# Kernel tuning notes

Measured on AMD Instinct MI355X. Metric: run time of the kernel, lower is better.

The kernel has to match this reference:

```python
import jax, jax.numpy as jnp
import numpy as np

EPS = 1e-6
MAX_ITER = 3

def skew(w):
    z = jnp.zeros_like(w[:, 0])
    return jnp.stack([
        jnp.stack([z, -w[:, 2], w[:, 1]], -1),
        jnp.stack([w[:, 2], z, -w[:, 0]], -1),
        jnp.stack([-w[:, 1], w[:, 0], z], -1)], -2)

def twist2mat(w):
    # Rodrigues formula, w: [B,3] -> R: [B,3,3]
    theta = jnp.linalg.norm(w, axis=-1, keepdims=True) + 1e-12
    axis = w / theta
    Km = skew(axis)
    th = theta[..., None]
    I = jnp.eye(3, dtype=w.dtype)
    return I + jnp.sin(th) * Km + (1.0 - jnp.cos(th)) * (Km @ Km)

def sobel_gradient(img, normalize=True):
    # replicate-pad + 3x3 Sobel, img: [B,C,H,W]
    p = jnp.pad(img, ((0, 0), (0, 0), (1, 1), (1, 1)), mode='edge')
    tl = p[..., :-2, :-2]; tc = p[..., :-2, 1:-1]; tr = p[..., :-2, 2:]
    ml = p[..., 1:-1, :-2]; mr = p[..., 1:-1, 2:]
    bl = p[..., 2:, :-2]; bc = p[..., 2:, 1:-1]; br = p[..., 2:, 2:]
    dx = (tr - tl) + 2.0 * (mr - ml) + (br - bl)
    dy = (bl - tl) + 2.0 * (bc - tc) + (br - tr)
    if normalize:
        mag = jnp.sqrt(dx * dx + dy * dy + 1e-8)
        dx, dy = dx / mag, dy / mag
    return dx, dy

def _bilinear_one(F, u, v):
    # F: [C,H,W]; u,v: [H,W] pixel coords; border padding (grid_sample-like)
    C, H, W = F.shape
    u = jnp.clip(u, 0.0, W - 1.0)
    v = jnp.clip(v, 0.0, H - 1.0)
    x0 = jnp.floor(u); y0 = jnp.floor(v)
    wx = u - x0; wy = v - y0
    x0i = x0.astype(jnp.int32); y0i = y0.astype(jnp.int32)
    x1i = jnp.minimum(x0i + 1, W - 1); y1i = jnp.minimum(y0i + 1, H - 1)
    g = lambda yi, xi: F[:, yi, xi]  # advanced-index gather -> [C,H,W]
    return (g(y0i, x0i) * (1 - wx) * (1 - wy) + g(y0i, x1i) * wx * (1 - wy)
            + g(y1i, x0i) * (1 - wx) * wy + g(y1i, x1i) * wx * wy)

def warp_features(F, u, v):
    # F: [B,C,H,W]; u,v: [B,1,H,W]
    return jax.vmap(_bilinear_one)(F, u[:, 0], v[:, 0])

def generate_xy_grid(B, H, W, K):
    fx, fy, cx, cy = [K[:, i].reshape(B, 1, 1, 1) for i in range(4)]
    uu, vv = jnp.meshgrid(jnp.arange(W, dtype=K.dtype), jnp.arange(H, dtype=K.dtype))
    px = (uu[None, None] - cx) / fx
    py = (vv[None, None] - cy) / fy
    return px, py  # [B,1,H,W] each

def batch_warp_inverse_depth(px, py, invD0, R, t, K):
    B, _, H, W = px.shape
    xy1 = jnp.concatenate([px, py, jnp.ones_like(px)], 1).reshape(B, 3, -1)
    warped = R @ xy1 + t[:, :, None] * invD0.reshape(B, 1, -1)
    x_, y_, s_ = warped[:, 0], warped[:, 1], warped[:, 2]
    fx, fy, cx, cy = [K[:, i].reshape(B, 1) for i in range(4)]
    u_ = (x_ / s_ * fx + cx).reshape(B, 1, H, W)
    v_ = (y_ / s_ * fy + cy).reshape(B, 1, H, W)
    inv_z = invD0 / s_.reshape(B, 1, H, W)
    return u_, v_, inv_z

def check_occ(inv_z_buffer, invD1, u, v, thres=0.1):
    B, _, H, W = invD1.shape
    inv_z_warped = warp_features(invD1, u, v)
    inlier = inv_z_buffer > inv_z_warped - thres
    inview = (u > 0) & (u < W) & (v > 0) & (v < H)
    return ~(inlier & inview)  # [B,1,H,W] bool

def compute_jacobian_warping(invD, K, px, py):
    # linearized at origin (pose=None branch)
    B, _, H, W = invD.shape
    x = px.reshape(B, -1); y = py.reshape(B, -1); d = invD.reshape(B, -1)
    O = jnp.zeros_like(x)
    xy = x * y
    dx_dp = jnp.stack([-xy, 1.0 + x * x, -y, d, O, -d * x], -1)
    dy_dp = jnp.stack([-(1.0 + y * y), xy, x, O, d, -d * y], -1)
    fx = K[:, 0].reshape(B, 1, 1); fy = K[:, 1].reshape(B, 1, 1)
    return dx_dp * fx, dy_dp * fy  # [B,HW,6] each

def lev_mar_H(JtWJ):
    diag = jnp.eye(6, dtype=JtWJ.dtype)
    trace = jnp.trace(JtWJ, axis1=1, axis2=2)
    return JtWJ + (trace * 1e-6)[:, None, None] * diag

def forward(twist0, x0, x1, invD0, invD1, sigma0, sigma1, K):
    B, C, H, W = x0.shape
    N = H * W
    dtype = x0.dtype
    R = twist2mat(twist0[:, :3])
    t = twist0[:, 3:]
    px, py = generate_xy_grid(B, H, W, K)
    # inverse-compositional: template Jacobian precomputed once
    Jf_x, Jf_y = sobel_gradient(x0, normalize=True)
    Jx_p, Jy_p = compute_jacobian_warping(invD0, K, px, py)
    J = (Jf_x.reshape(B, C, N, 1) * Jx_p.reshape(B, 1, N, 6)
         + Jf_y.reshape(B, C, N, 1) * Jy_p.reshape(B, 1, N, 6))  # [B,C,N,6]
    for _ in range(MAX_ITER):
        u_w, v_w, inv_z = batch_warp_inverse_depth(px, py, invD0, R, t, K)
        occ = check_occ(inv_z, invD1, u_w, v_w)
        f_r = warp_features(x1, u_w, v_w)
        sigma_r = warp_features(sigma1, u_w, v_w)
        res = f_r - x0
        sigma = jnp.sqrt(sigma_r * sigma_r + sigma0 * sigma0)
        wres = jnp.where(occ, EPS, res / sigma)  # [B,C,H,W]
        valid = (~occ).reshape(B, 1, N, 1).astype(dtype)
        Jw = (J / sigma.reshape(B, C, N, 1) * valid).reshape(B, C * N, 6)
        r = jnp.where(occ, 0.0, wres).reshape(B, C * N)
        JtWJ = jnp.einsum('bnk,bnl->bkl', Jw, Jw)
        Rhs = jnp.einsum('bnk,bn->bk', Jw, r)[..., None]
        xi = jnp.linalg.solve(lev_mar_H(JtWJ), Rhs)  # [B,6,1]
        d_R = twist2mat(-xi[:, :3, 0])
        d_t = -(d_R @ xi[:, 3:])
        t = (R @ d_t)[:, :, 0] + t
        R = R @ d_R
    return jnp.concatenate([R.reshape(B, 9), t], axis=1)  # [B,12]

def setup_inputs() -> dict:
    key = jax.random.key(0)
    ks = jax.random.split(key, 7)
    B, C, H, W = 8, 16, 240, 320
    twist0 = jax.random.normal(ks[0], (B, 6), jnp.float32) * 0.01
    x0 = jax.random.normal(ks[1], (B, C, H, W), jnp.float32)
    x1 = jax.random.normal(ks[2], (B, C, H, W), jnp.float32)
    invD0 = jax.random.uniform(ks[3], (B, 1, H, W), jnp.float32, 0.1, 1.0)
    invD1 = jax.random.uniform(ks[4], (B, 1, H, W), jnp.float32, 0.1, 1.0)
    sigma0 = jax.random.uniform(ks[5], (B, C, H, W), jnp.float32, 0.1, 1.0)
    sigma1 = jax.random.uniform(ks[6], (B, C, H, W), jnp.float32, 0.1, 1.0)
    Kmat = jnp.tile(jnp.array([[0.8 * W, 0.8 * W, W / 2.0, H / 2.0]], jnp.float32), (B, 1))
    return dict(twist0=twist0, x0=x0, x1=x1, invD0=invD0, invD1=invD1,
                sigma0=sigma0, sigma1=sigma1, K=Kmat)

def reference(twist0, x0, x1, invD0, invD1, sigma0, sigma1, K):
    return forward(twist0, x0, x1, invD0, invD1, sigma0, sigma1, K)
```

## Files before the change

### kernel.cpp

```cpp
#include <hip/hip_runtime.h>
#include <hip/hip_fp16.h>

#define B_ 8
#define C_ 16
#define H_ 240
#define W_ 320
#define N_ (H_*W_)

__device__ __forceinline__ void twist2mat_dev(float w0, float w1, float w2, float R[9]) {
    float th = sqrtf(w0*w0 + w1*w1 + w2*w2) + 1e-12f;
    float ax = w0/th, ay = w1/th, az = w2/th;
    float s = sinf(th), c = cosf(th), ic = 1.0f - c;
    R[0] = 1.0f + ic*(ax*ax - 1.0f);
    R[1] = -s*az + ic*ax*ay;
    R[2] =  s*ay + ic*ax*az;
    R[3] =  s*az + ic*ax*ay;
    R[4] = 1.0f + ic*(ay*ay - 1.0f);
    R[5] = -s*ax + ic*ay*az;
    R[6] = -s*ay + ic*ax*az;
    R[7] =  s*ax + ic*ay*az;
    R[8] = 1.0f + ic*(az*az - 1.0f);
}

__device__ __forceinline__ unsigned pack_h2(float a, float b) {
    __half2 h = __floats2half2_rn(a, b);
    return *reinterpret_cast<unsigned*>(&h);
}
__device__ __forceinline__ float2 unpack_h2(unsigned u) {
    __half2 h = *reinterpret_cast<__half2*>(&u);
    return __half22float2(h);
}

__device__ __forceinline__ void solve_update(const float* __restrict__ ac, float R[9], float t[3]) {
    float M[6][7];
    {
        int idx = 0;
        #pragma unroll
        for (int k = 0; k < 6; k++)
            #pragma unroll
            for (int l = k; l < 6; l++) { M[k][l] = ac[idx]; M[l][k] = ac[idx]; idx++; }
    }
    const float trace = M[0][0]+M[1][1]+M[2][2]+M[3][3]+M[4][4]+M[5][5];
    const float lam = trace * 1e-6f;
    #pragma unroll
    for (int i = 0; i < 6; i++) { M[i][i] += lam; M[i][6] = ac[21+i]; }

    #pragma unroll
    for (int k = 0; k < 6; k++) {
        const float inv = 1.0f / M[k][k];
        #pragma unroll
        for (int i = k+1; i < 6; i++) {
            const float f = M[i][k] * inv;
            #pragma unroll
            for (int j = k; j < 7; j++) M[i][j] -= f * M[k][j];
        }
    }
    float xi[6];
    #pragma unroll
    for (int i = 5; i >= 0; i--) {
        float s = M[i][6];
        #pragma unroll
        for (int j = i+1; j < 6; j++) s -= M[i][j]*xi[j];
        xi[i] = s / M[i][i];
    }

    float dR[9];
    twist2mat_dev(-xi[0], -xi[1], -xi[2], dR);
    const float dt0 = -(dR[0]*xi[3] + dR[1]*xi[4] + dR[2]*xi[5]);
    const float dt1 = -(dR[3]*xi[3] + dR[4]*xi[4] + dR[5]*xi[5]);
    const float dt2 = -(dR[6]*xi[3] + dR[7]*xi[4] + dR[8]*xi[5]);

    const float nt0 = R[0]*dt0 + R[1]*dt1 + R[2]*dt2 + t[0];
    const float nt1 = R[3]*dt0 + R[4]*dt1 + R[5]*dt2 + t[1];
    const float nt2 = R[6]*dt0 + R[7]*dt1 + R[8]*dt2 + t[2];
    float nR[9];
    #pragma unroll
    for (int i = 0; i < 3; i++)
        #pragma unroll
        for (int j = 0; j < 3; j++)
            nR[i*3+j] = R[i*3+0]*dR[0*3+j] + R[i*3+1]*dR[1*3+j] + R[i*3+2]*dR[2*3+j];
    #pragma unroll
    for (int i = 0; i < 9; i++) R[i] = nR[i];
    t[0] = nt0; t[1] = nt1; t[2] = nt2;
}

__device__ __forceinline__ void build_RT(const float* __restrict__ twist0,
                                         const float* __restrict__ accum,
                                         int b, int iters, float R[9], float t[3]) {
    const float* w = twist0 + b*6;
    twist2mat_dev(w[0], w[1], w[2], R);
    t[0] = w[3]; t[1] = w[4]; t[2] = w[5];
    for (int j = 0; j < iters; j++)
        solve_update(accum + (size_t)(j*B_ + b)*27, R, t);
}

__launch_bounds__(256)
__global__ void precompute_kernel(const float* __restrict__ x0, const float* __restrict__ x1,
                                  const float* __restrict__ sigma0, const float* __restrict__ sigma1,
                                  uint4* __restrict__ P0h, uint4* __restrict__ X1S1h,
                                  float* __restrict__ accum)
{
    if (blockIdx.x == 0 && blockIdx.y == 0 && blockIdx.z == 0) {
        for (int k = threadIdx.x; k < 3*B_*27; k += 256) accum[k] = 0.0f;
    }
    const int p4 = blockIdx.x*256 + threadIdx.x;
    const int pix = p4 * 4;
    const int cg = blockIdx.y;
    const int b  = blockIdx.z;
    const int h = pix / W_;
    const int w = pix - h*W_;
    const int hm = max(h-1,0), hp = min(h+1,H_-1);
    const int wl = max(w-1,0), wr = min(w+4,W_-1);

    unsigned gw[4][4], xw[4][4], qw[4][4];

    #pragma unroll
    for (int i = 0; i < 4; i++) {
        const int c = cg*4 + i;
        const size_t base = ((size_t)(b*C_+c))*N_;
        const float* xc = x0 + base;
        const float4 rt = *reinterpret_cast<const float4*>(xc + hm*W_ + w);
        const float4 rm = *reinterpret_cast<const float4*>(xc + h *W_ + w);
        const float4 rb = *reinterpret_cast<const float4*>(xc + hp*W_ + w);
        const float T[6]  = { xc[hm*W_+wl], rt.x, rt.y, rt.z, rt.w, xc[hm*W_+wr] };
        const float Mw[6] = { xc[h *W_+wl], rm.x, rm.y, rm.z, rm.w, xc[h *W_+wr] };
        const float Bo[6] = { xc[hp*W_+wl], rb.x, rb.y, rb.z, rb.w, xc[hp*W_+wr] };
        const float4 s0v = *reinterpret_cast<const float4*>(sigma0 + base + pix);
        const float4 x1v = *reinterpret_cast<const float4*>(x1 + base + pix);
        const float4 s1v = *reinterpret_cast<const float4*>(sigma1 + base + pix);
        const float s0a[4] = {s0v.x, s0v.y, s0v.z, s0v.w};
        const float x1a[4] = {x1v.x, x1v.y, x1v.z, x1v.w};
        const float s1a[4] = {s1v.x, s1v.y, s1v.z, s1v.w};
        #pragma unroll
        for (int j = 0; j < 4; j++) {
            const float dx = T[j+2] - T[j] + 2.0f*(Mw[j+2] - Mw[j]) + (Bo[j+2] - Bo[j]);
            const float dy = Bo[j] - T[j] + 2.0f*(Bo[j+1] - T[j+1]) + (Bo[j+2] - T[j+2]);
            const float mag = sqrtf(dx*dx + dy*dy + 1e-8f);
            gw[i][j] = pack_h2(dx/mag, dy/mag);
            xw[i][j] = pack_h2(Mw[j+1], s0a[j]*s0a[j]);
            qw[i][j] = pack_h2(x1a[j], s1a[j]);
        }
    }
    uint4* PA = P0h + ((size_t)(b*8 + cg*2  ))*N_ + pix;
    uint4* PB = P0h + ((size_t)(b*8 + cg*2+1))*N_ + pix;
    uint4* Qp = X1S1h + ((size_t)(b*4 + cg))*N_ + pix;
    #pragma unroll
    for (int j = 0; j < 4; j++) {
        uint4 a;  a.x = gw[0][j];  a.y = xw[0][j];  a.z = gw[1][j];  a.w = xw[1][j];
        uint4 bb; bb.x = gw[2][j]; bb.y = xw[2][j]; bb.z = gw[3][j]; bb.w = xw[3][j];
        uint4 q;  q.x = qw[0][j];  q.y = qw[1][j];  q.z = qw[2][j];  q.w = qw[3][j];
        PA[j] = a; PB[j] = bb; Qp[j] = q;
    }
}

__device__ __forceinline__ void accum_pixel(int pix,
                                            const float Rm[9], const float tv[3],
                                            float fx, float fy, float cx, float cy,
                                            const uint4* __restrict__ P0b,
                                            const uint4* __restrict__ X1S1b,
                                            const float* __restrict__ d0,
                                            const float* __restrict__ dz,
                                            float* __restrict__ acc)
{
    const int h = pix / W_;
    const int w = pix - h*W_;

    const float px = ((float)w - cx) / fx;
    const float py = ((float)h - cy) / fy;
    const float d  = d0[pix];

    const float x_ = Rm[0]*px + Rm[1]*py + Rm[2] + tv[0]*d;
    const float y_ = Rm[3]*px + Rm[4]*py + Rm[5] + tv[1]*d;
    const float s_ = Rm[6]*px + Rm[7]*py + Rm[8] + tv[2]*d;
    const float u = x_/s_*fx + cx;
    const float v = y_/s_*fy + cy;
    const float inv_z = d / s_;

    const float uc = fminf(fmaxf(u, 0.0f), (float)(W_-1));
    const float vc = fminf(fmaxf(v, 0.0f), (float)(H_-1));
    const float x0f = floorf(uc), y0f = floorf(vc);
    const float wx = uc - x0f, wy = vc - y0f;
    const int x0i = (int)x0f, y0i = (int)y0f;
    const int x1i = min(x0i+1, W_-1), y1i = min(y0i+1, H_-1);
    const float w00 = (1.0f-wx)*(1.0f-wy), w01 = wx*(1.0f-wy);
    const float w10 = (1.0f-wx)*wy,        w11 = wx*wy;
    const int i00 = y0i*W_+x0i, i01 = y0i*W_+x1i, i10 = y1i*W_+x0i, i11 = y1i*W_+x1i;

    const float zw = dz[i00]*w00 + dz[i01]*w01 + dz[i10]*w10 + dz[i11]*w11;
    const bool inlier = inv_z > zw - 0.1f;
    const bool inview = (u > 0.0f) && (u < (float)W_) && (v > 0.0f) && (v < (float)H_);
    const bool valid  = inlier && inview;

    if (!valid) return;

    const float xy = px*py;
    const float Av[6] = { -xy*fx, (1.0f+px*px)*fx, -py*fx, d*fx, 0.0f, -d*px*fx };
    const float Bv[6] = { -(1.0f+py*py)*fy, xy*fy, px*fy, 0.0f, d*fy, -d*py*fy };

    float Swxx=0.f, Swxy=0.f, Swyy=0.f, Srx=0.f, Sry=0.f;

#define CH(gword, xword, t00, t01, t10, t11) { \
    const float2 g  = unpack_h2(gword); \
    const float2 xs = unpack_h2(xword); \
    const float2 a00 = unpack_h2(t00), a01 = unpack_h2(t01), \
                 a10 = unpack_h2(t10), a11 = unpack_h2(t11); \
    const float fr = a00.x*w00 + a01.x*w01 + a10.x*w10 + a11.x*w11; \
    const float sr = a00.y*w00 + a01.y*w01 + a10.y*w10 + a11.y*w11; \
    const float inv_s2 = 1.0f/(sr*sr + xs.y); \
    const float res = fr - xs.x; \
    const float gxw = g.x*inv_s2, gyw = g.y*inv_s2; \
    Swxx += g.x*gxw; Swxy += g.x*gyw; Swyy += g.y*gyw; \
    Srx  += res*gxw; Sry  += res*gyw; }

    #pragma unroll
    for (int cg = 0; cg < 4; cg++) {
        const uint4 pA = P0b[(size_t)(cg*2  )*N_ + pix];
        const uint4 pB = P0b[(size_t)(cg*2+1)*N_ + pix];
        const uint4* xsb = X1S1b + (size_t)cg*N_;
        const uint4 q00 = xsb[i00], q01 = xsb[i01], q10 = xsb[i10], q11 = xsb[i11];
        CH(pA.x, pA.y, q00.x, q01.x, q10.x, q11.x)
        CH(pA.z, pA.w, q00.y, q01.y, q10.y, q11.y)
        CH(pB.x, pB.y, q00.z, q01.z, q10.z, q11.z)
        CH(pB.z, pB.w, q00.w, q01.w, q10.w, q11.w)
    }
#undef CH

    int idx = 0;
    #pragma unroll
    for (int k = 0; k < 6; k++) {
        #pragma unroll
        for (int l = k; l < 6; l++) {
            acc[idx++] += Swxx*Av[k]*Av[l] + Swxy*(Av[k]*Bv[l] + Bv[k]*Av[l]) + Swyy*Bv[k]*Bv[l];
        }
    }
    #pragma unroll
    for (int k = 0; k < 6; k++) acc[21+k] += Srx*Av[k] + Sry*Bv[k];
}

__launch_bounds__(256)
__global__ void iter_kernel(const uint4* __restrict__ P0h, const uint4* __restrict__ X1S1h,
                            const float* __restrict__ invD0, const float* __restrict__ invD1,
                            const float* __restrict__ Kmat, const float* __restrict__ twist0,
                            float* __restrict__ accum, int it)
{
    const int b = blockIdx.y;
    const int pix0 = blockIdx.x * 512 + threadIdx.x;

    float Rm[9], tv[3];
    build_RT(twist0, accum, b, it, Rm, tv);

    const float fx = Kmat[b*4+0], fy = Kmat[b*4+1], cx = Kmat[b*4+2], cy = Kmat[b*4+3];

    float acc[27];
    #pragma unroll
    for (int j = 0; j < 27; j++) acc[j] = 0.0f;

    const uint4* P0b   = P0h   + (size_t)b*8*N_;
    const uint4* X1S1b = X1S1h + (size_t)b*4*N_;
    const float* d0 = invD0 + b*N_;
    const float* dz = invD1 + b*N_;

    accum_pixel(pix0,       Rm, tv, fx, fy, cx, cy, P0b, X1S1b, d0, dz, acc);
    accum_pixel(pix0 + 256, Rm, tv, fx, fy, cx, cy, P0b, X1S1b, d0, dz, acc);

    const int lane = threadIdx.x & 63;
    const int wave = threadIdx.x >> 6;
    __shared__ float red[4][27];
    #pragma unroll
    for (int j = 0; j < 27; j++) {
        float vv = acc[j];
        vv += __shfl_down(vv, 32);
        vv += __shfl_down(vv, 16);
        vv += __shfl_down(vv, 8);
        vv += __shfl_down(vv, 4);
        vv += __shfl_down(vv, 2);
        vv += __shfl_down(vv, 1);
        if (lane == 0) red[wave][j] = vv;
    }
    __syncthreads();
    if (threadIdx.x < 27) {
        float s = red[0][threadIdx.x] + red[1][threadIdx.x] + red[2][threadIdx.x] + red[3][threadIdx.x];
        atomicAdd(&accum[(size_t)(it*B_ + b)*27 + threadIdx.x], s);
    }
}

__global__ void finalize_kernel(const float* __restrict__ twist0, const float* __restrict__ accum,
                                float* __restrict__ out)
{
    const int b = threadIdx.x;
    if (b >= B_) return;
    float Rm[9], tv[3];
    build_RT(twist0, accum, b, 3, Rm, tv);
    float* ob = out + b*12;
    #pragma unroll
    for (int i = 0; i < 9; i++) ob[i] = Rm[i];
    ob[9] = tv[0]; ob[10] = tv[1]; ob[11] = tv[2];
}

extern "C" void kernel_launch(void* const* d_in, const int* in_sizes, int n_in,
                              void* d_out, int out_size, void* d_ws, size_t ws_size,
                              hipStream_t stream) {
    const float* twist0 = (const float*)d_in[0];
    const float* x0     = (const float*)d_in[1];
    const float* x1     = (const float*)d_in[2];
    const float* invD0  = (const float*)d_in[3];
    const float* invD1  = (const float*)d_in[4];
    const float* sigma0 = (const float*)d_in[5];
    const float* sigma1 = (const float*)d_in[6];
    const float* Kmat   = (const float*)d_in[7];
    float* out = (float*)d_out;

    const size_t p0_bytes = (size_t)B_*8*N_*sizeof(uint4);
    const size_t xs_bytes = (size_t)B_*4*N_*sizeof(uint4);

    uint4* P0h   = (uint4*)d_ws;
    uint4* X1S1h = (uint4*)((char*)d_ws + p0_bytes);
    float* accum = (float*)((char*)d_ws + p0_bytes + xs_bytes);

    hipLaunchKernelGGL(precompute_kernel, dim3(N_/(256*4), 4, B_), dim3(256), 0, stream,
                       x0, x1, sigma0, sigma1, P0h, X1S1h, accum);

    dim3 grid(N_/512, B_);
    for (int it = 0; it < 3; ++it) {
        hipLaunchKernelGGL(iter_kernel, grid, dim3(256), 0, stream,
                           P0h, X1S1h, invD0, invD1, Kmat, twist0, accum, it);
    }
    hipLaunchKernelGGL(finalize_kernel, dim3(1), dim3(64), 0, stream, twist0, accum, out);
}
```

Baseline: 363.9 us.

## Stage x0 stencil rows in LDS and process one pixel per thread in precompute

The precompute kernel now loads the rows of x0 that a block needs (one row above, one below, four channels) into shared memory with float4 loads, then computes the Sobel stencil from LDS, one pixel per thread. This replaces the unaligned scalar halo loads and repeated global reads of neighbouring rows with coalesced loads and on-chip reuse. The grid grows fourfold and each thread's stores become single strided uint4 writes. A block of 256 pixels can straddle a row boundary, which is why four rows are staged instead of three.

```diff
diff --git a/kernel.cpp b/kernel.cpp
--- a/kernel.cpp
+++ b/kernel.cpp
@@ -103,54 +103,67 @@
     if (blockIdx.x == 0 && blockIdx.y == 0 && blockIdx.z == 0) {
         for (int k = threadIdx.x; k < 3*B_*27; k += 256) accum[k] = 0.0f;
     }
-    const int p4 = blockIdx.x*256 + threadIdx.x;
-    const int pix = p4 * 4;
+    const int b  = blockIdx.z;
     const int cg = blockIdx.y;
-    const int b  = blockIdx.z;
+    const int base_pix = blockIdx.x * 256;
+    const int pix = base_pix + threadIdx.x;
+    const int h0 = base_pix / W_;
+
+    __shared__ float lds[4][4][W_];
+
+    const size_t cbase = ((size_t)(b*C_) + cg*4) * N_;
+
+    float s0a[4], x1a[4], s1a[4];
+    #pragma unroll
+    for (int i = 0; i < 4; i++) {
+        const size_t o = cbase + (size_t)i*N_ + pix;
+        s0a[i] = sigma0[o];
+        x1a[i] = x1[o];
+        s1a[i] = sigma1[o];
+    }
+
+    #pragma unroll
+    for (int k = 0; k < 5; k++) {
+        const int idx = threadIdx.x + k*256;
+        const int ch  = idx / 320;
+        const int rem = idx - ch*320;
+        const int row = rem / 80;
+        const int c4  = rem - row*80;
+        const int src_r = min(max(h0 - 1 + row, 0), H_ - 1);
+        const float4 v = *reinterpret_cast<const float4*>(
+            x0 + cbase + (size_t)ch*N_ + (size_t)src_r*W_ + c4*4);
+        *reinterpret_cast<float4*>(&lds[ch][row][c4*4]) = v;
+    }
+    __syncthreads();
+
     const int h = pix / W_;
     const int w = pix - h*W_;
-    const int hm = max(h-1,0), hp = min(h+1,H_-1);
-    const int wl = max(w-1,0), wr = min(w+4,W_-1);
-
-    unsigned gw[4][4], xw[4][4], qw[4][4];
-
+    const int lr = h - (h0 - 1);
+    const int wm = max(w-1, 0), wp = min(w+1, W_-1);
+
+    unsigned gq[4], xq[4], qq[4];
     #pragma unroll
     for (int i = 0; i < 4; i++) {
-        const int c = cg*4 + i;
-        const size_t base = ((size_t)(b*C_+c))*N_;
-        const float* xc = x0 + base;
-        const float4 rt = *reinterpret_cast<const float4*>(xc + hm*W_ + w);
-        const float4 rm = *reinterpret_cast<const float4*>(xc + h *W_ + w);
-        const float4 rb = *reinterpret_cast<const float4*>(xc + hp*W_ + w);
-        const float T[6]  = { xc[hm*W_+wl], rt.x, rt.y, rt.z, rt.w, xc[hm*W_+wr] };
-        const float Mw[6] = { xc[h *W_+wl], rm.x, rm.y, rm.z, rm.w, xc[h *W_+wr] };
-        const float Bo[6] = { xc[hp*W_+wl], rb.x, rb.y, rb.z, rb.w, xc[hp*W_+wr] };
-        const float4 s0v = *reinterpret_cast<const float4*>(sigma0 + base + pix);
-        const float4 x1v = *reinterpret_cast<const float4*>(x1 + base + pix);
-        const float4 s1v = *reinterpret_cast<const float4*>(sigma1 + base + pix);
-        const float s0a[4] = {s0v.x, s0v.y, s0v.z, s0v.w};
-        const float x1a[4] = {x1v.x, x1v.y, x1v.z, x1v.w};
-        const float s1a[4] = {s1v.x, s1v.y, s1v.z, s1v.w};
-        #pragma unroll
-        for (int j = 0; j < 4; j++) {
-            const float dx = T[j+2] - T[j] + 2.0f*(Mw[j+2] - Mw[j]) + (Bo[j+2] - Bo[j]);
-            const float dy = Bo[j] - T[j] + 2.0f*(Bo[j+1] - T[j+1]) + (Bo[j+2] - T[j+2]);
-            const float mag = sqrtf(dx*dx + dy*dy + 1e-8f);
-            gw[i][j] = pack_h2(dx/mag, dy/mag);
-            xw[i][j] = pack_h2(Mw[j+1], s0a[j]*s0a[j]);
-            qw[i][j] = pack_h2(x1a[j], s1a[j]);
-        }
-    }
-    uint4* PA = P0h + ((size_t)(b*8 + cg*2  ))*N_ + pix;
-    uint4* PB = P0h + ((size_t)(b*8 + cg*2+1))*N_ + pix;
-    uint4* Qp = X1S1h + ((size_t)(b*4 + cg))*N_ + pix;
-    #pragma unroll
-    for (int j = 0; j < 4; j++) {
-        uint4 a;  a.x = gw[0][j];  a.y = xw[0][j];  a.z = gw[1][j];  a.w = xw[1][j];
-        uint4 bb; bb.x = gw[2][j]; bb.y = xw[2][j]; bb.z = gw[3][j]; bb.w = xw[3][j];
-        uint4 q;  q.x = qw[0][j];  q.y = qw[1][j];  q.z = qw[2][j];  q.w = qw[3][j];
-        PA[j] = a; PB[j] = bb; Qp[j] = q;
-    }
+        const float* rT = lds[i][lr-1];
+        const float* rM = lds[i][lr];
+        const float* rB = lds[i][lr+1];
+        const float tl = rT[wm], tc_ = rT[w], tr = rT[wp];
+        const float ml = rM[wm], ctr = rM[w], mr = rM[wp];
+        const float bl = rB[wm], bc_ = rB[w], br = rB[wp];
+        const float dx = tr - tl + 2.0f*(mr - ml) + (br - bl);
+        const float dy = bl - tl + 2.0f*(bc_ - tc_) + (br - tr);
+        const float mag = sqrtf(dx*dx + dy*dy + 1e-8f);
+        gq[i] = pack_h2(dx/mag, dy/mag);
+        xq[i] = pack_h2(ctr, s0a[i]*s0a[i]);
+        qq[i] = pack_h2(x1a[i], s1a[i]);
+    }
+
+    uint4 A;  A.x = gq[0];  A.y = xq[0];  A.z = gq[1];  A.w = xq[1];
+    uint4 Bw; Bw.x = gq[2]; Bw.y = xq[2]; Bw.z = gq[3]; Bw.w = xq[3];
+    uint4 Q;  Q.x = qq[0];  Q.y = qq[1];  Q.z = qq[2];  Q.w = qq[3];
+    P0h[((size_t)(b*8 + cg*2  ))*N_ + pix] = A;
+    P0h[((size_t)(b*8 + cg*2+1))*N_ + pix] = Bw;
+    X1S1h[((size_t)(b*4 + cg))*N_ + pix] = Q;
 }
 
 __device__ __forceinline__ void accum_pixel(int pix,
@@ -317,7 +330,7 @@
     uint4* X1S1h = (uint4*)((char*)d_ws + p0_bytes);
     float* accum = (float*)((char*)d_ws + p0_bytes + xs_bytes);
 
-    hipLaunchKernelGGL(precompute_kernel, dim3(N_/(256*4), 4, B_), dim3(256), 0, stream,
+    hipLaunchKernelGGL(precompute_kernel, dim3(N_/256, 4, B_), dim3(256), 0, stream,
                        x0, x1, sigma0, sigma1, P0h, X1S1h, accum);
 
     dim3 grid(N_/512, B_);
```

New measurement: 335.6 us. 7.8% less time.
